# Kernel tuning notes

Hardware: AMD Instinct MI355X
Metric: run time of the kernel (lower is better)

## Reference

```python
import jax, jax.numpy as jnp
import numpy as np

B, H, L, D = 4, 4096, 8, 64  # queries shape [B, L, H, D]
FACTOR = 5
U = FACTOR * int(np.ceil(np.log(4096)))  # u_part = u = 45 (L_q == L_k)


def setup_inputs() -> dict:
    key = jax.random.key(0)
    kq, kk, kv, ki = jax.random.split(key, 4)
    queries = jax.random.normal(kq, (4, 4096, 8, 64), dtype=jnp.float32)
    keys = jax.random.normal(kk, (4, 4096, 8, 64), dtype=jnp.float32)
    values = jax.random.normal(kv, (4, 4096, 8, 64), dtype=jnp.float32)
    index_sample = jax.random.randint(ki, (4096, U), 0, 4096)  # torch.randint(key_length,(L_Q,sample_k))
    return {"queries": queries, "keys": keys, "values": values, "index_sample": index_sample}


def reference(queries, keys, values, index_sample):
    # (B, L, H, D) -> (B, H, L, D)
    q = jnp.transpose(queries, (0, 2, 1, 3))
    k = jnp.transpose(keys, (0, 2, 1, 3))
    v = jnp.transpose(values, (0, 2, 1, 3))
    b, h, l_q, d = q.shape
    l_k = k.shape[2]
    n_top = index_sample.shape[1]  # u == u_part == 45 here

    # --- _prob_QK: sampled QK scores (avoid materializing key_expand [B,H,Lq,Lk,D]) ---
    # key_sample: [B, H, Lq, sample_k, D]
    key_sample = k[:, :, index_sample, :]
    # Q_i . K_sampled: [B, H, Lq, sample_k]
    qk_sample = jnp.einsum('bhld,bhlsd->bhls', q, key_sample)
    # sparsity measure M = max - mean(over full key_length)
    m = jnp.max(qk_sample, axis=-1) - jnp.sum(qk_sample, axis=-1) / l_k  # [B,H,Lq]
    _, m_top = jax.lax.top_k(m, n_top)  # [B, H, u]

    # reduced queries: [B, H, u, D]
    q_reduce = jnp.take_along_axis(q, m_top[..., None], axis=2)
    scores_top = jnp.einsum('bhud,bhkd->bhuk', q_reduce, k)  # [B, H, u, Lk]

    scale = 1.0 / jnp.sqrt(jnp.asarray(d, dtype=q.dtype))
    scores_top = scores_top * scale

    # --- _get_initial_context (mask_flag=False): mean of values broadcast over queries ---
    context = jnp.broadcast_to(jnp.mean(v, axis=2, keepdims=True), (b, h, l_q, d))

    # --- _update_context: softmax + scatter attn@V into the top-u query rows ---
    attn = jax.nn.softmax(scores_top, axis=-1)  # [B, H, u, Lk]
    update = jnp.einsum('bhuk,bhkd->bhud', attn, v)  # [B, H, u, D]
    b_idx = jnp.arange(b)[:, None, None]
    h_idx = jnp.arange(h)[None, :, None]
    context = context.at[b_idx, h_idx, m_top].set(update)
    return context  # [B, H, Lq, D]
```

## Files before the change

kernel.cpp:

```cpp
#include <hip/hip_runtime.h>
#include <hip/hip_bf16.h>


#define NB 4
#define NH 8
#define NL 4096
#define ND 64
#define NS 45
#define SCALE 0.125f
#define NCHUNK 16
#define CHUNK 256

typedef float floatx4 __attribute__((ext_vector_type(4)));

static __device__ __forceinline__ float neg_inf() { return -__builtin_inff(); }

template <int CTRL>
static __device__ __forceinline__ float dpp_add(float x) {
  int y = __builtin_amdgcn_update_dpp(0, __builtin_bit_cast(int, x), CTRL,
                                      0xF, 0xF, true);
  return x + __builtin_bit_cast(float, y);
}
static __device__ __forceinline__ float red16(float x) {
  x = dpp_add<0x140>(x);
  x = dpp_add<0x141>(x);
  x = dpp_add<0x4E>(x);
  x = dpp_add<0xB1>(x);
  return x;
}
static __device__ __forceinline__ float red4(float x) {
  x = dpp_add<0xB1>(x);
  x = dpp_add<0x4E>(x);
  return x;
}

template <int BS>
static __device__ __forceinline__ void batch_dot(
    const float* __restrict__ kbase, const int* __restrict__ srow, int s0,
    floatx4 qr, int lane, float& mx, float& sm) {
  floatx4 kr[BS];
#pragma unroll
  for (int j = 0; j < BS; j++) {
    int ki = __builtin_amdgcn_readfirstlane(srow[s0 + j]);
    kr[j] = *((const floatx4*)(kbase + (size_t)ki * 512) + lane);
  }
  float p[BS];
#pragma unroll
  for (int j = 0; j < BS; j++) {
    float d = kr[j].x * qr.x + kr[j].y * qr.y + kr[j].z * qr.z + kr[j].w * qr.w;
    p[j] = red16(d);
  }
#pragma unroll
  for (int j = 0; j < BS; j++) { mx = fmaxf(mx, p[j]); sm += p[j]; }
}

__global__ __launch_bounds__(512) void kA_m_meanv(
    const float* __restrict__ q, const float* __restrict__ k,
    const float* __restrict__ v, const int* __restrict__ idxs,
    float* __restrict__ m_out, float* __restrict__ vpart)
{
  __shared__ int sidx[4][48];
  __shared__ float lmx[8][4], lsm[8][4];
  __shared__ float part[8][ND];
  int gb = blockIdx.x;
  int t = threadIdx.x, w = t >> 6, lane = t & 63, g = lane >> 4;

  if (gb < 8192) {
    int pair = gb & 7;
    int b = pair >> 1, hg = pair & 1;
    int lg = gb >> 3;
    int wl = w & 3;
    int l = lg * 4 + wl;

    if (w < 4 && lane < NS) sidx[w][lane] = idxs[l * NS + lane];

    const floatx4* q4 =
        (const floatx4*)(q + ((size_t)(b * NL + l) * NH + hg * 4) * ND);
    floatx4 qr = __builtin_nontemporal_load(q4 + lane);
    const float* kbase = k + ((size_t)b * NL * NH + hg * 4) * ND;
    const int* srow = sidx[wl];
    __syncthreads();

    float mx = neg_inf(), sm = 0.f;
    if (w < 4) {
      batch_dot<8>(kbase, srow, 0, qr, lane, mx, sm);
      batch_dot<8>(kbase, srow, 8, qr, lane, mx, sm);
      batch_dot<8>(kbase, srow, 16, qr, lane, mx, sm);
    } else {
      batch_dot<7>(kbase, srow, 24, qr, lane, mx, sm);
      batch_dot<7>(kbase, srow, 31, qr, lane, mx, sm);
      batch_dot<7>(kbase, srow, 38, qr, lane, mx, sm);
    }
    if ((lane & 15) == 0) { lmx[w][g] = mx; lsm[w][g] = sm; }
    __syncthreads();
    if (w < 4 && (lane & 15) == 0) {
      float MX = fmaxf(lmx[w][g], lmx[w + 4][g]);
      float SM = lsm[w][g] + lsm[w + 4][g];
      m_out[((size_t)b * NH + hg * 4 + g) * NL + l] = MX - SM * (1.0f / 4096.0f);
    }
  } else {
    int idx = gb - 8192;
    int bh = idx >> 5, cc = idx & 31;
    int b = bh >> 3, h = bh & 7;
    int d = t & 63, gg = t >> 6;
    float a0 = 0.f, a1 = 0.f, a2 = 0.f, a3 = 0.f;
    const float* vb = v + ((size_t)(b * NL + cc * 128) * NH + h) * ND + d;
#pragma unroll
    for (int i = 0; i < 4; i++) {
      a0 += vb[(size_t)(gg + 8 * (4 * i + 0)) * NH * ND];
      a1 += vb[(size_t)(gg + 8 * (4 * i + 1)) * NH * ND];
      a2 += vb[(size_t)(gg + 8 * (4 * i + 2)) * NH * ND];
      a3 += vb[(size_t)(gg + 8 * (4 * i + 3)) * NH * ND];
    }
    part[gg][d] = (a0 + a1) + (a2 + a3);
    __syncthreads();
    if (gg == 0) {
      float s = 0.f;
#pragma unroll
      for (int j = 0; j < 8; j++) s += part[j][d];
      vpart[(bh * 32 + cc) * ND + d] = s;
    }
  }
}

__global__ __launch_bounds__(256) void k_topk_p1(
    const float* __restrict__ m_in, unsigned long long* __restrict__ cand)
{
  __shared__ unsigned long long keys[512];
  __shared__ unsigned long long wred[4];
  int blk = blockIdx.x;
  int bh = blk >> 3, slice = blk & 7;
  int t = threadIdx.x, wid = t >> 6, lane = t & 63;
  int base = slice * 512;
  for (int i = t; i < 512; i += 256) {
    float v = m_in[bh * NL + base + i];
    unsigned u = __float_as_uint(v);
    u ^= (u >> 31) ? 0xFFFFFFFFu : 0x80000000u;
    keys[i] = ((unsigned long long)u << 32) | (unsigned)(~(unsigned)(base + i));
  }
  __syncthreads();
  for (int it = 0; it < NS; ++it) {
    unsigned long long k0 = keys[t], k1 = keys[t + 256];
    unsigned long long best = k0 > k1 ? k0 : k1;
#pragma unroll
    for (int off = 32; off; off >>= 1) {
      unsigned long long o = __shfl_xor(best, off);
      if (o > best) best = o;
    }
    if (lane == 0) wred[wid] = best;
    __syncthreads();
    if (t == 0) {
      unsigned long long b0 = wred[0];
      if (wred[1] > b0) b0 = wred[1];
      if (wred[2] > b0) b0 = wred[2];
      if (wred[3] > b0) b0 = wred[3];
      cand[blk * NS + it] = b0;
      int gi = (int)(~(unsigned)(b0 & 0xFFFFFFFFull));
      keys[gi - base] = 0;
    }
    __syncthreads();
  }
}

__global__ __launch_bounds__(256) void kC_topk2_meanv(
    const unsigned long long* __restrict__ cand, int* __restrict__ mtop,
    const float* __restrict__ vpart, float* __restrict__ meanv)
{
  __shared__ unsigned long long keys[8 * NS];
  __shared__ unsigned long long wred[4];
  __shared__ unsigned long long sbest;
  __shared__ float part2[4][ND];
  int gb = blockIdx.x;
  int t = threadIdx.x, wid = t >> 6, lane = t & 63;

  if (gb < 32) {
    int bh = gb;
    for (int i = t; i < 8 * NS; i += 256) keys[i] = cand[bh * 8 * NS + i];
    __syncthreads();
    for (int it = 0; it < NS; ++it) {
      unsigned long long best = (t < 8 * NS) ? keys[t] : 0ull;
      if (t + 256 < 8 * NS) {
        unsigned long long k1 = keys[t + 256];
        if (k1 > best) best = k1;
      }
#pragma unroll
      for (int off = 32; off; off >>= 1) {
        unsigned long long o = __shfl_xor(best, off);
        if (o > best) best = o;
      }
      if (lane == 0) wred[wid] = best;
      __syncthreads();
      if (t == 0) {
        unsigned long long b0 = wred[0];
        if (wred[1] > b0) b0 = wred[1];
        if (wred[2] > b0) b0 = wred[2];
        if (wred[3] > b0) b0 = wred[3];
        sbest = b0;
        mtop[bh * NS + it] = (int)(~(unsigned)(b0 & 0xFFFFFFFFull));
      }
      __syncthreads();
      unsigned long long bb = sbest;
      if (t < 8 * NS && keys[t] == bb) keys[t] = 0;
      if (t + 256 < 8 * NS && keys[t + 256] == bb) keys[t + 256] = 0;
      __syncthreads();
    }
  } else {
    int bh = gb - 32;
    int d = t & 63, gg = t >> 6;
    float s = 0.f;
#pragma unroll
    for (int i = 0; i < 8; i++) s += vpart[(bh * 32 + gg + 4 * i) * ND + d];
    part2[gg][d] = s;
    __syncthreads();
    if (gg == 0) {
      float tot = part2[0][d] + part2[1][d] + part2[2][d] + part2[3][d];
      meanv[bh * ND + d] = tot * (1.0f / 4096.0f);
    }
  }
}

__global__ __launch_bounds__(1024) void kD_scores_fill(
    const float* __restrict__ q, const float* __restrict__ k,
    const float* __restrict__ v, const int* __restrict__ mtop,
    const float* __restrict__ meanv,
    float* __restrict__ mc_out, float* __restrict__ lc_out,
    float* __restrict__ op_out, float4* __restrict__ out4)
{
  __shared__ float QLDS[NS * ND];
  __shared__ float SLDS[NS * 260];
  __shared__ int mt[NS];
  __shared__ float mcs[NS], lcs[NS];

  int gb = blockIdx.x;
  int t = threadIdx.x;
  int wid = t >> 6, lane = t & 63;

  if (gb >= 512) {
    const int total = NB * NH * NL * ND / 4;
    const float4* mv4 = (const float4*)meanv;
    for (int i = (gb - 512) * 1024 + t; i < total; i += 512 * 1024) {
      int bh = i >> 16;
      out4[i] = mv4[bh * 16 + (i & 15)];
    }
    return;
  }

  int xcd = gb & 7, seq = gb >> 3;
  int bh = xcd * 4 + (seq >> 4);
  int c = seq & 15;
  int b = bh >> 3, h = bh & 7;

  if (t < NS) mt[t] = mtop[bh * NS + t];
  __syncthreads();

  const float4* q4 = (const float4*)q;
  float4* QL4 = (float4*)QLDS;
  if (t < NS * 16) {
    int u = t >> 4, j = t & 15;
    QL4[t] = q4[((size_t)(b * NL + mt[u]) * NH + h) * 16 + j];
  }
  __syncthreads();

  {
    int kk = wid * 16 + (lane >> 2);
    int seg = lane & 3;
    const float4* k4 =
        (const float4*)(k + ((size_t)(b * NL + c * CHUNK + kk) * NH + h) * ND)
        + seg * 4;
    float4 k0 = k4[0], k1 = k4[1], k2 = k4[2], k3 = k4[3];
    const float4* qp = QL4 + seg * 4;
    for (int u = 0; u < NS; ++u) {
      float4 a0 = qp[u * 16 + 0], a1 = qp[u * 16 + 1];
      float4 a2 = qp[u * 16 + 2], a3 = qp[u * 16 + 3];
      float dot = a0.x * k0.x + a0.y * k0.y + a0.z * k0.z + a0.w * k0.w
                + a1.x * k1.x + a1.y * k1.y + a1.z * k1.z + a1.w * k1.w
                + a2.x * k2.x + a2.y * k2.y + a2.z * k2.z + a2.w * k2.w
                + a3.x * k3.x + a3.y * k3.y + a3.z * k3.z + a3.w * k3.w;
      dot = red4(dot);
      if (seg == 0) SLDS[u * 260 + kk] = dot * SCALE;
    }
  }
  __syncthreads();

  for (int u = wid; u < NS; u += 16) {
    float4 sv = *(const float4*)&SLDS[u * 260 + lane * 4];
    float mx = fmaxf(fmaxf(sv.x, sv.y), fmaxf(sv.z, sv.w));
#pragma unroll
    for (int off = 32; off; off >>= 1) mx = fmaxf(mx, __shfl_xor(mx, off));
    float e0 = expf(sv.x - mx), e1 = expf(sv.y - mx);
    float e2 = expf(sv.z - mx), e3 = expf(sv.w - mx);
    float s = e0 + e1 + e2 + e3;
#pragma unroll
    for (int off = 32; off; off >>= 1) s += __shfl_xor(s, off);
    *(float4*)&SLDS[u * 260 + lane * 4] = make_float4(e0, e1, e2, e3);
    if (lane == 0) { mcs[u] = mx; lcs[u] = s; }
  }
  __syncthreads();

  float acc[3];
#pragma unroll
  for (int i = 0; i < 3; i++) acc[i] = 0.f;
  const float* vbase = v + ((size_t)(b * NL + c * CHUNK) * NH + h) * ND + lane;
  for (int kb = 0; kb < 64; ++kb) {
    float vd0 = vbase[(size_t)(kb * 4 + 0) * NH * ND];
    float vd1 = vbase[(size_t)(kb * 4 + 1) * NH * ND];
    float vd2 = vbase[(size_t)(kb * 4 + 2) * NH * ND];
    float vd3 = vbase[(size_t)(kb * 4 + 3) * NH * ND];
#pragma unroll
    for (int i = 0; i < 3; i++) {
      int u = wid + 16 * i;
      if (u < NS) {
        float4 p4 = *(const float4*)&SLDS[u * 260 + kb * 4];
        acc[i] += p4.x * vd0 + p4.y * vd1 + p4.z * vd2 + p4.w * vd3;
      }
    }
  }
#pragma unroll
  for (int i = 0; i < 3; i++) {
    int u = wid + 16 * i;
    if (u < NS)
      op_out[(((size_t)bh * NCHUNK + c) * NS + u) * ND + lane] = acc[i];
  }
  if (t < NS) {
    mc_out[(bh * NCHUNK + c) * NS + t] = mcs[t];
    lc_out[(bh * NCHUNK + c) * NS + t] = lcs[t];
  }
}

__global__ __launch_bounds__(256) void k_combine(
    const float* __restrict__ mc, const float* __restrict__ lc,
    const float* __restrict__ op, const int* __restrict__ mtop,
    float* __restrict__ out)
{
  int gw = blockIdx.x * 4 + (threadIdx.x >> 6);
  int lane = threadIdx.x & 63;
  int bh = gw / NS, u = gw % NS;
  float M = neg_inf();
  for (int c = 0; c < NCHUNK; c++)
    M = fmaxf(M, mc[(bh * NCHUNK + c) * NS + u]);
  float Lsum = 0.f, O = 0.f;
  for (int c = 0; c < NCHUNK; c++) {
    float e = expf(mc[(bh * NCHUNK + c) * NS + u] - M);
    Lsum += lc[(bh * NCHUNK + c) * NS + u] * e;
    O += op[(((size_t)bh * NCHUNK + c) * NS + u) * ND + lane] * e;
  }
  int row = mtop[bh * NS + u];
  out[((size_t)bh * NL + row) * ND + lane] = O / Lsum;
}

extern "C" void kernel_launch(void* const* d_in, const int* in_sizes, int n_in,
                              void* d_out, int out_size, void* d_ws, size_t ws_size,
                              hipStream_t stream) {
  const float* q = (const float*)d_in[0];
  const float* k = (const float*)d_in[1];
  const float* v = (const float*)d_in[2];
  const int* idxs = (const int*)d_in[3];
  float* out = (float*)d_out;
  float* ws = (float*)d_ws;

  float* m_ws  = ws;
  int*   mtop  = (int*)(ws + 131072);
  float* meanv = ws + 132512;
  float* mc    = ws + 134560;
  float* lc    = ws + 157600;
  float* op    = ws + 180640;
  float* vpart = op;
  unsigned long long* cand = (unsigned long long*)(op + 131072);

  hipLaunchKernelGGL(kA_m_meanv,     dim3(8192 + 1024), dim3(512),  0, stream,
                     q, k, v, idxs, m_ws, vpart);
  hipLaunchKernelGGL(k_topk_p1,      dim3(256),         dim3(256),  0, stream,
                     m_ws, cand);
  hipLaunchKernelGGL(kC_topk2_meanv, dim3(64),          dim3(256),  0, stream,
                     cand, mtop, vpart, meanv);
  hipLaunchKernelGGL(kD_scores_fill, dim3(1024),        dim3(1024), 0, stream,
                     q, k, v, mtop, meanv, mc, lc, op, (float4*)out);
  hipLaunchKernelGGL(k_combine,      dim3(360),         dim3(256),  0, stream,
                     mc, lc, op, mtop, out);
}
```

Measured before the change: 177.3 us.

## Shrink sampled-QK blocks to one wave per query and use nontemporal fill stores

The sampled-score kernel drops from 512 to 256 threads. Each wave now handles all 45 sampled keys for its query in a loop of 9-key batches. This removes the cross-wave split, the LDS max/sum merge and its two barriers. The mean-V partial blocks are resized to 256 threads over 64-row chunks, which doubles the partial count and the reduction loop in the top-k kernel. The broadcast fill of the output now uses nontemporal stores to avoid polluting cache. The cost is fewer loads in flight per query row and a serial loop of 5 batches per wave.

Measured after the change: 176.3 us. About the same (-0.6%).

```diff
diff --git a/kernel.cpp b/kernel.cpp
--- a/kernel.cpp
+++ b/kernel.cpp
@@ -34,34 +34,13 @@
   return x;
 }
 
-template <int BS>
-static __device__ __forceinline__ void batch_dot(
-    const float* __restrict__ kbase, const int* __restrict__ srow, int s0,
-    floatx4 qr, int lane, float& mx, float& sm) {
-  floatx4 kr[BS];
-#pragma unroll
-  for (int j = 0; j < BS; j++) {
-    int ki = __builtin_amdgcn_readfirstlane(srow[s0 + j]);
-    kr[j] = *((const floatx4*)(kbase + (size_t)ki * 512) + lane);
-  }
-  float p[BS];
-#pragma unroll
-  for (int j = 0; j < BS; j++) {
-    float d = kr[j].x * qr.x + kr[j].y * qr.y + kr[j].z * qr.z + kr[j].w * qr.w;
-    p[j] = red16(d);
-  }
-#pragma unroll
-  for (int j = 0; j < BS; j++) { mx = fmaxf(mx, p[j]); sm += p[j]; }
-}
-
-__global__ __launch_bounds__(512) void kA_m_meanv(
+__global__ __launch_bounds__(256) void kA_m_meanv(
     const float* __restrict__ q, const float* __restrict__ k,
     const float* __restrict__ v, const int* __restrict__ idxs,
     float* __restrict__ m_out, float* __restrict__ vpart)
 {
   __shared__ int sidx[4][48];
-  __shared__ float lmx[8][4], lsm[8][4];
-  __shared__ float part[8][ND];
+  __shared__ float part[4][ND];
   int gb = blockIdx.x;
   int t = threadIdx.x, w = t >> 6, lane = t & 63, g = lane >> 4;
 
@@ -69,56 +48,59 @@
     int pair = gb & 7;
     int b = pair >> 1, hg = pair & 1;
     int lg = gb >> 3;
-    int wl = w & 3;
-    int l = lg * 4 + wl;
-
-    if (w < 4 && lane < NS) sidx[w][lane] = idxs[l * NS + lane];
+    int l = lg * 4 + w;
+
+    if (lane < NS) sidx[w][lane] = idxs[l * NS + lane];
 
     const floatx4* q4 =
         (const floatx4*)(q + ((size_t)(b * NL + l) * NH + hg * 4) * ND);
     floatx4 qr = __builtin_nontemporal_load(q4 + lane);
     const float* kbase = k + ((size_t)b * NL * NH + hg * 4) * ND;
-    const int* srow = sidx[wl];
-    __syncthreads();
 
     float mx = neg_inf(), sm = 0.f;
-    if (w < 4) {
-      batch_dot<8>(kbase, srow, 0, qr, lane, mx, sm);
-      batch_dot<8>(kbase, srow, 8, qr, lane, mx, sm);
-      batch_dot<8>(kbase, srow, 16, qr, lane, mx, sm);
-    } else {
-      batch_dot<7>(kbase, srow, 24, qr, lane, mx, sm);
-      batch_dot<7>(kbase, srow, 31, qr, lane, mx, sm);
-      batch_dot<7>(kbase, srow, 38, qr, lane, mx, sm);
-    }
-    if ((lane & 15) == 0) { lmx[w][g] = mx; lsm[w][g] = sm; }
-    __syncthreads();
-    if (w < 4 && (lane & 15) == 0) {
-      float MX = fmaxf(lmx[w][g], lmx[w + 4][g]);
-      float SM = lsm[w][g] + lsm[w + 4][g];
-      m_out[((size_t)b * NH + hg * 4 + g) * NL + l] = MX - SM * (1.0f / 4096.0f);
-    }
+#pragma unroll 1
+    for (int s0 = 0; s0 < NS; s0 += 9) {
+      floatx4 kr[9];
+#pragma unroll
+      for (int j = 0; j < 9; j++) {
+        int ki = __builtin_amdgcn_readfirstlane(sidx[w][s0 + j]);
+        kr[j] = *((const floatx4*)(kbase + (size_t)ki * 512) + lane);
+      }
+      float p[9];
+#pragma unroll
+      for (int j = 0; j < 9; j++) {
+        float d = kr[j].x * qr.x + kr[j].y * qr.y + kr[j].z * qr.z +
+                  kr[j].w * qr.w;
+        p[j] = red16(d);
+      }
+      float m0 = fmaxf(fmaxf(p[0], p[1]), p[2]);
+      float m1 = fmaxf(fmaxf(p[3], p[4]), p[5]);
+      float m2 = fmaxf(fmaxf(p[6], p[7]), p[8]);
+      mx = fmaxf(fmaxf(mx, m0), fmaxf(m1, m2));
+      sm += ((p[0] + p[1]) + (p[2] + p[3])) +
+            ((p[4] + p[5]) + (p[6] + p[7])) + p[8];
+    }
+    if ((lane & 15) == 0)
+      m_out[((size_t)b * NH + hg * 4 + g) * NL + l] = mx - sm * (1.0f / 4096.0f);
   } else {
     int idx = gb - 8192;
-    int bh = idx >> 5, cc = idx & 31;
+    int bh = idx >> 6, c = idx & 63;
     int b = bh >> 3, h = bh & 7;
     int d = t & 63, gg = t >> 6;
     float a0 = 0.f, a1 = 0.f, a2 = 0.f, a3 = 0.f;
-    const float* vb = v + ((size_t)(b * NL + cc * 128) * NH + h) * ND + d;
+    const float* vb = v + ((size_t)(b * NL + c * 64) * NH + h) * ND + d;
 #pragma unroll
     for (int i = 0; i < 4; i++) {
-      a0 += vb[(size_t)(gg + 8 * (4 * i + 0)) * NH * ND];
-      a1 += vb[(size_t)(gg + 8 * (4 * i + 1)) * NH * ND];
-      a2 += vb[(size_t)(gg + 8 * (4 * i + 2)) * NH * ND];
-      a3 += vb[(size_t)(gg + 8 * (4 * i + 3)) * NH * ND];
+      a0 += vb[(size_t)(gg + 4 * (4 * i + 0)) * NH * ND];
+      a1 += vb[(size_t)(gg + 4 * (4 * i + 1)) * NH * ND];
+      a2 += vb[(size_t)(gg + 4 * (4 * i + 2)) * NH * ND];
+      a3 += vb[(size_t)(gg + 4 * (4 * i + 3)) * NH * ND];
     }
     part[gg][d] = (a0 + a1) + (a2 + a3);
     __syncthreads();
     if (gg == 0) {
-      float s = 0.f;
-#pragma unroll
-      for (int j = 0; j < 8; j++) s += part[j][d];
-      vpart[(bh * 32 + cc) * ND + d] = s;
+      float s = part[0][d] + part[1][d] + part[2][d] + part[3][d];
+      vpart[(bh * 64 + c) * ND + d] = s;
     }
   }
 }
@@ -209,7 +191,7 @@
     int d = t & 63, gg = t >> 6;
     float s = 0.f;
 #pragma unroll
-    for (int i = 0; i < 8; i++) s += vpart[(bh * 32 + gg + 4 * i) * ND + d];
+    for (int i = 0; i < 16; i++) s += vpart[(bh * 64 + gg + 4 * i) * ND + d];
     part2[gg][d] = s;
     __syncthreads();
     if (gg == 0) {
@@ -224,7 +206,7 @@
     const float* __restrict__ v, const int* __restrict__ mtop,
     const float* __restrict__ meanv,
     float* __restrict__ mc_out, float* __restrict__ lc_out,
-    float* __restrict__ op_out, float4* __restrict__ out4)
+    float* __restrict__ op_out, float* __restrict__ out)
 {
   __shared__ float QLDS[NS * ND];
   __shared__ float SLDS[NS * 260];
@@ -237,10 +219,11 @@
 
   if (gb >= 512) {
     const int total = NB * NH * NL * ND / 4;
-    const float4* mv4 = (const float4*)meanv;
+    const floatx4* mv4 = (const floatx4*)meanv;
+    floatx4* o4 = (floatx4*)out;
     for (int i = (gb - 512) * 1024 + t; i < total; i += 512 * 1024) {
       int bh = i >> 16;
-      out4[i] = mv4[bh * 16 + (i & 15)];
+      __builtin_nontemporal_store(mv4[bh * 16 + (i & 15)], o4 + i);
     }
     return;
   }
@@ -367,14 +350,14 @@
   float* vpart = op;
   unsigned long long* cand = (unsigned long long*)(op + 131072);
 
-  hipLaunchKernelGGL(kA_m_meanv,     dim3(8192 + 1024), dim3(512),  0, stream,
+  hipLaunchKernelGGL(kA_m_meanv,     dim3(8192 + 2048), dim3(256),  0, stream,
                      q, k, v, idxs, m_ws, vpart);
   hipLaunchKernelGGL(k_topk_p1,      dim3(256),         dim3(256),  0, stream,
                      m_ws, cand);
   hipLaunchKernelGGL(kC_topk2_meanv, dim3(64),          dim3(256),  0, stream,
                      cand, mtop, vpart, meanv);
   hipLaunchKernelGGL(kD_scores_fill, dim3(1024),        dim3(1024), 0, stream,
-                     q, k, v, mtop, meanv, mc, lc, op, (float4*)out);
+                     q, k, v, mtop, meanv, mc, lc, op, out);
   hipLaunchKernelGGL(k_combine,      dim3(360),         dim3(256),  0, stream,
                      mc, lc, op, mtop, out);
 }
```
